# Kernel optimization log

Hardware: AMD Instinct MI355X
Metric: run time of the kernel (lower is better)

Reference implementation:

```python
import jax, jax.numpy as jnp
import numpy as np

B, T, C = 4, 4096, 1024
HEAD_SIZE = 64
HEAD_OUT = 64


def setup_inputs() -> dict:
    key = jax.random.key(0)
    kx, kk, kq, kv = jax.random.split(key, 4)
    x = jax.random.normal(kx, (B, T, C), dtype=jnp.float32)
    # nn.Linear(in, out, bias=False): weight [out, in]; y = x @ W.T
    Wk = jax.random.normal(kk, (HEAD_SIZE, C), dtype=jnp.float32) * (C ** -0.5)
    Wq = jax.random.normal(kq, (HEAD_SIZE, C), dtype=jnp.float32) * (C ** -0.5)
    Wv = jax.random.normal(kv, (HEAD_OUT, C), dtype=jnp.float32) * (C ** -0.5)
    return {"x": x, "Wk": Wk, "Wq": Wq, "Wv": Wv}


def reference(x, Wk, Wq, Wv):
    Tlen = x.shape[1]
    k = jnp.einsum('btc,hc->bth', x, Wk)  # [B,T,Hs]
    q = jnp.einsum('btc,hc->bth', x, Wq)  # [B,T,Hs]
    v = jnp.einsum('btc,oc->bto', x, Wv)  # [B,T,Ho]
    scale = HEAD_SIZE ** -0.5
    scores = jnp.einsum('bih,bjh->bij', q, k) * scale  # [B,T,T]
    # torch.tril(ones, diagonal=1): allowed where j <= i+1 (note: one superdiagonal kept)
    i = jnp.arange(Tlen)[:, None]
    j = jnp.arange(Tlen)[None, :]
    allowed = j <= i + 1
    masked = jnp.where(allowed, scores, -jnp.inf)
    # NOTE: original scales AGAIN inside softmax (double scaling, faithful)
    weights = jax.nn.softmax(masked * scale, axis=-1)
    return jnp.einsum('bij,bjo->bio', weights, v)  # [B,T,Ho]
```

## Files before the change

### kernel.cpp

```cpp
#include <hip/hip_runtime.h>

#define BB 4
#define TT 4096
#define CC 1024
#define HH 64
#define AW 4

typedef unsigned short us;
typedef us v8u __attribute__((ext_vector_type(8)));
typedef us v4u __attribute__((ext_vector_type(4)));
typedef __bf16 v8bf __attribute__((ext_vector_type(8)));
typedef float v4f __attribute__((ext_vector_type(4)));

__device__ __forceinline__ us f2bf(float f) {
  unsigned u = __builtin_bit_cast(unsigned, f);
  u += 0x7fffu + ((u >> 16) & 1u);
  return (us)(u >> 16);
}
__device__ __forceinline__ v8bf ldb(const us* p) {
  return __builtin_bit_cast(v8bf, *(const v8u*)p);
}

__global__ __launch_bounds__(256) void convertw_kernel(const float* __restrict__ Wk,
                                                       const float* __restrict__ Wq,
                                                       const float* __restrict__ Wv,
                                                       us* __restrict__ wpack) {
  const int g = blockIdx.x * 256 + threadIdx.x;
  const int t = g >> 13;
  const int rem = g & 8191;
  const int oc = rem >> 11;
  const int kc = (rem >> 6) & 31;
  const int lane = rem & 63;
  const float* W = (t == 0) ? Wq : ((t == 1) ? Wk : Wv);
  const int h  = oc * 16 + (lane & 15);
  const int d0 = kc * 32 + (lane >> 4) * 8;
  const float4* src = (const float4*)(W + h * CC + d0);
  const float4 f0 = src[0], f1 = src[1];
  v8u o;
  o[0]=f2bf(f0.x); o[1]=f2bf(f0.y); o[2]=f2bf(f0.z); o[3]=f2bf(f0.w);
  o[4]=f2bf(f1.x); o[5]=f2bf(f1.y); o[6]=f2bf(f1.z); o[7]=f2bf(f1.w);
  *(v8u*)(wpack + (size_t)g * 8) = o;
}


__global__ __launch_bounds__(512, 4) void proj_kernel(
    const float* __restrict__ x, const us* __restrict__ wpack,
    us* __restrict__ qpack, us* __restrict__ kpack, us* __restrict__ vpack)
{
  __shared__ __align__(16) float red[3][2][3][4][64][4];

  const int tid  = threadIdx.x;
  const int lane = tid & 63, w = tid >> 6;
  const int i16 = lane & 15, quad = lane >> 4;
  const int rg = w & 1, kq = w >> 1;
  const int rows0 = blockIdx.x * 32;

  const float* xp = x + (size_t)(rows0 + rg * 16 + i16) * CC + kq * 256 + quad * 8;

  v4f zero = {0.f, 0.f, 0.f, 0.f};
  v4f acc[3][4];
  #pragma unroll
  for (int t = 0; t < 3; t++)
    #pragma unroll
    for (int oc = 0; oc < 4; oc++) acc[t][oc] = zero;

  #pragma unroll 2
  for (int kc = 0; kc < 8; kc++) {
    const float4 f0 = *(const float4*)(xp + kc * 32);
    const float4 f1 = *(const float4*)(xp + kc * 32 + 4);
    v8u au;
    au[0]=f2bf(f0.x); au[1]=f2bf(f0.y); au[2]=f2bf(f0.z); au[3]=f2bf(f0.w);
    au[4]=f2bf(f1.x); au[5]=f2bf(f1.y); au[6]=f2bf(f1.z); au[7]=f2bf(f1.w);
    const v8bf a = __builtin_bit_cast(v8bf, au);
    const size_t wo = (size_t)(kq * 8 + kc) * 512 + lane * 8;
    #pragma unroll
    for (int oc = 0; oc < 4; oc++) {
      acc[0][oc] = __builtin_amdgcn_mfma_f32_16x16x32_bf16(a, ldb(wpack + (0*4+oc)*16384 + wo), acc[0][oc], 0, 0, 0);
      acc[1][oc] = __builtin_amdgcn_mfma_f32_16x16x32_bf16(a, ldb(wpack + (1*4+oc)*16384 + wo), acc[1][oc], 0, 0, 0);
      acc[2][oc] = __builtin_amdgcn_mfma_f32_16x16x32_bf16(a, ldb(wpack + (2*4+oc)*16384 + wo), acc[2][oc], 0, 0, 0);
    }
  }

  if (kq) {
    #pragma unroll
    for (int t = 0; t < 3; t++)
      #pragma unroll
      for (int oc = 0; oc < 4; oc++)
        *(v4f*)&red[kq - 1][rg][t][oc][lane][0] = acc[t][oc];
  }
  __syncthreads();

  if (kq == 0) {
    #pragma unroll
    for (int p = 0; p < 3; p++)
      #pragma unroll
      for (int t = 0; t < 3; t++)
        #pragma unroll
        for (int oc = 0; oc < 4; oc++) {
          const v4f pv = *(const v4f*)&red[p][rg][t][oc][lane][0];
          #pragma unroll
          for (int r = 0; r < 4; r++) acc[t][oc][r] += pv[r];
        }

    const float COEF = 0.015625f * 1.4426950408889634f;
    const int b    = (rows0 >> 12);
    const int tile = (rows0 & (TT - 1)) >> 5;

    #pragma unroll
    for (int oc = 0; oc < 4; oc++) {
      const int h = oc * 16 + i16;
      #pragma unroll
      for (int r = 0; r < 4; r++) {
        const int tr = quad * 4 + r;
        const int lane2 = tr + 16 * ((h >> 3) & 3);
        const size_t idx = ((((size_t)(b * 128 + tile) * 2 + rg) * 2 + (h >> 5)) * 64 + lane2) * 8 + (h & 7);
        qpack[idx] = f2bf(acc[0][oc][r] * COEF);
        kpack[idx] = f2bf(acc[1][oc][r]);
      }
      const int lane3 = i16 + 16 * (rg * 2 + (quad >> 1));
      v4u pk;
      #pragma unroll
      for (int r = 0; r < 4; r++) pk[r] = f2bf(acc[2][oc][r]);
      *(v4u*)&vpack[(((size_t)(b * 128 + tile) * 4 + oc) * 64 + lane3) * 8 + (quad & 1) * 4] = pk;
    }
  }
}

__global__ __launch_bounds__(256) void attn_kernel(
    const us* __restrict__ qpack, const us* __restrict__ kpack,
    const us* __restrict__ vpack, float* __restrict__ out)
{
  __shared__ float shbuf[AW][2148];

  const int tid  = threadIdx.x;
  const int lane = tid & 63, warp = tid >> 6;
  const int i16 = lane & 15, quad = lane >> 4;

  const int p = blockIdx.x & 255, s = blockIdx.x >> 8;
  const int b  = p & 3;
  const int q0 = p >> 2;
  const int qb = s ? (127 - q0) : q0;
  const int i0 = qb << 5;
  const int nt = min(qb + 2, 128);

  us* Pw = (us*)shbuf[warp];
  const float NEGINF = -__builtin_inff();

  v8bf qf[2][2];
  #pragma unroll
  for (int ih = 0; ih < 2; ih++)
    #pragma unroll
    for (int g = 0; g < 2; g++)
      qf[ih][g] = ldb(qpack + ((((size_t)(b * 128 + qb) * 2 + ih) * 2 + g) * 64 + lane) * 8);

  v4f zero = {0.f, 0.f, 0.f, 0.f};
  v4f oacc[2][4];
  #pragma unroll
  for (int ih = 0; ih < 2; ih++)
    #pragma unroll
    for (int oc = 0; oc < 4; oc++) oacc[ih][oc] = zero;
  float lsum[2] = {0.f, 0.f};

  auto loadK = [&](int t, v8bf kf[2][2]) {
    #pragma unroll
    for (int f = 0; f < 2; f++)
      #pragma unroll
      for (int g = 0; g < 2; g++)
        kf[f][g] = ldb(kpack + ((((size_t)(b * 128 + t) * 2 + f) * 2 + g) * 64 + lane) * 8);
  };
  auto loadV = [&](int t, v8bf vf[4]) {
    #pragma unroll
    for (int oc = 0; oc < 4; oc++)
      vf[oc] = ldb(vpack + (((size_t)(b * 128 + t) * 4 + oc) * 64 + lane) * 8);
  };
  auto qk_exp_store = [&](int t, const v8bf kf[2][2], int buf) {
    v4f sacc[2][2];
    #pragma unroll
    for (int ih = 0; ih < 2; ih++)
      #pragma unroll
      for (int f = 0; f < 2; f++) {
        v4f sv = zero;
        sv = __builtin_amdgcn_mfma_f32_16x16x32_bf16(kf[f][0], qf[ih][0], sv, 0, 0, 0);
        sv = __builtin_amdgcn_mfma_f32_16x16x32_bf16(kf[f][1], qf[ih][1], sv, 0, 0, 0);
        sacc[ih][f] = sv;
      }
    const int j0 = t * 32;
    const bool needMask = (t >= qb);
    #pragma unroll
    for (int ih = 0; ih < 2; ih++) {
      float ps[8];
      #pragma unroll
      for (int f = 0; f < 2; f++)
        #pragma unroll
        for (int r = 0; r < 4; r++) {
          float sv = fminf(sacc[ih][f][r], 80.f);
          if (needMask) {
            const int j = j0 + f * 16 + quad * 4 + r;
            const int i = i0 + ih * 16 + i16;
            sv = (j <= i + 1) ? sv : NEGINF;
          }
          ps[f * 4 + r] = exp2f(sv);
          lsum[ih] += ps[f * 4 + r];
        }
      #pragma unroll
      for (int f = 0; f < 2; f++) {
        v4u pk;
        #pragma unroll
        for (int r = 0; r < 4; r++) pk[r] = f2bf(ps[f * 4 + r]);
        *(v4u*)&Pw[buf * 1280 + ih * 640 + i16 * 40 + f * 16 + quad * 4] = pk;
      }
    }
  };
  auto pv = [&](int buf, const v8bf vf[4]) {
    #pragma unroll
    for (int ih = 0; ih < 2; ih++) {
      v8bf pf = __builtin_bit_cast(v8bf, *(const v8u*)&Pw[buf * 1280 + ih * 640 + i16 * 40 + quad * 8]);
      #pragma unroll
      for (int oc = 0; oc < 4; oc++)
        oacc[ih][oc] = __builtin_amdgcn_mfma_f32_16x16x32_bf16(vf[oc], pf, oacc[ih][oc], 0, 0, 0);
    }
  };

  int t = warp, buf = 0;
  if (t < nt) {
    v8bf kf[2][2], vprev[4];
    loadK(t, kf); loadV(t, vprev);
    qk_exp_store(t, kf, 0);
    for (t += AW; t < nt; t += AW) {
      v8bf kf2[2][2], vnew[4];
      loadK(t, kf2); loadV(t, vnew);
      pv(buf, vprev);
      qk_exp_store(t, kf2, buf ^ 1);
      #pragma unroll
      for (int v = 0; v < 4; v++) vprev[v] = vnew[v];
      buf ^= 1;
    }
    pv(buf, vprev);
  }

  #pragma unroll
  for (int ih = 0; ih < 2; ih++) {
    lsum[ih] += __shfl_xor(lsum[ih], 16, 64);
    lsum[ih] += __shfl_xor(lsum[ih], 32, 64);
    #pragma unroll
    for (int oc = 0; oc < 4; oc++)
      #pragma unroll
      for (int r = 0; r < 4; r++)
        shbuf[warp][(oc * 16 + quad * 4 + r) * 33 + ih * 16 + i16] = oacc[ih][oc][r];
  }
  if (lane < 16) {
    shbuf[warp][2112 + lane]      = lsum[0];
    shbuf[warp][2112 + 16 + lane] = lsum[1];
  }
  __syncthreads();

  const int o  = tid & 63;
  const int iw = tid >> 6;
  #pragma unroll
  for (int rr = 0; rr < 8; rr++) {
    const int i = iw + rr * 4;
    float L = 0.f, O = 0.f;
    #pragma unroll
    for (int w = 0; w < AW; w++) {
      L += shbuf[w][2112 + i];
      O += shbuf[w][o * 33 + i];
    }
    out[(size_t)(b * TT + i0 + i) * HH + o] = O / L;
  }
}

extern "C" void kernel_launch(void* const* d_in, const int* in_sizes, int n_in,
                              void* d_out, int out_size, void* d_ws, size_t ws_size,
                              hipStream_t stream) {
  const size_t NWP = 3 * 4 * 32 * 64 * 8;
  const size_t NP  = (size_t)BB * TT * HH;

  us* wpack = (us*)d_ws;
  us* qpack = wpack + NWP;
  us* kpack = qpack + NP;
  us* vpack = kpack + NP;
  float* out = (float*)d_out;

  convertw_kernel<<<96, 256, 0, stream>>>(
      (const float*)d_in[1], (const float*)d_in[2], (const float*)d_in[3], wpack);
  proj_kernel<<<BB * TT / 32, 512, 0, stream>>>(
      (const float*)d_in[0], wpack, qpack, kpack, vpack);
  attn_kernel<<<512, 256, 0, stream>>>(qpack, kpack, vpack, out);
}
```

Baseline: 157.4 us.

## Restructure projection to stage x tile in LDS and split outputs across warps

```diff
diff --git a/kernel.cpp b/kernel.cpp
--- a/kernel.cpp
+++ b/kernel.cpp
@@ -43,84 +43,74 @@
 }
 
 
-__global__ __launch_bounds__(512, 4) void proj_kernel(
+__global__ __launch_bounds__(768, 6) void proj_kernel(
     const float* __restrict__ x, const us* __restrict__ wpack,
     us* __restrict__ qpack, us* __restrict__ kpack, us* __restrict__ vpack)
 {
-  __shared__ __align__(16) float red[3][2][3][4][64][4];
+  __shared__ __align__(16) us xlds[64][520];
 
   const int tid  = threadIdx.x;
   const int lane = tid & 63, w = tid >> 6;
   const int i16 = lane & 15, quad = lane >> 4;
-  const int rg = w & 1, kq = w >> 1;
-  const int rows0 = blockIdx.x * 32;
-
-  const float* xp = x + (size_t)(rows0 + rg * 16 + i16) * CC + kq * 256 + quad * 8;
-
+  const int t = w >> 2, oc = w & 3;
+  const int rows0 = blockIdx.x * 64;
+
+  const us* wp = wpack + (size_t)w * 16384 + lane * 8;
   v4f zero = {0.f, 0.f, 0.f, 0.f};
-  v4f acc[3][4];
-  #pragma unroll
-  for (int t = 0; t < 3; t++)
-    #pragma unroll
-    for (int oc = 0; oc < 4; oc++) acc[t][oc] = zero;
-
-  #pragma unroll 2
-  for (int kc = 0; kc < 8; kc++) {
-    const float4 f0 = *(const float4*)(xp + kc * 32);
-    const float4 f1 = *(const float4*)(xp + kc * 32 + 4);
-    v8u au;
-    au[0]=f2bf(f0.x); au[1]=f2bf(f0.y); au[2]=f2bf(f0.z); au[3]=f2bf(f0.w);
-    au[4]=f2bf(f1.x); au[5]=f2bf(f1.y); au[6]=f2bf(f1.z); au[7]=f2bf(f1.w);
-    const v8bf a = __builtin_bit_cast(v8bf, au);
-    const size_t wo = (size_t)(kq * 8 + kc) * 512 + lane * 8;
-    #pragma unroll
-    for (int oc = 0; oc < 4; oc++) {
-      acc[0][oc] = __builtin_amdgcn_mfma_f32_16x16x32_bf16(a, ldb(wpack + (0*4+oc)*16384 + wo), acc[0][oc], 0, 0, 0);
-      acc[1][oc] = __builtin_amdgcn_mfma_f32_16x16x32_bf16(a, ldb(wpack + (1*4+oc)*16384 + wo), acc[1][oc], 0, 0, 0);
-      acc[2][oc] = __builtin_amdgcn_mfma_f32_16x16x32_bf16(a, ldb(wpack + (2*4+oc)*16384 + wo), acc[2][oc], 0, 0, 0);
-    }
-  }
-
-  if (kq) {
-    #pragma unroll
-    for (int t = 0; t < 3; t++)
-      #pragma unroll
-      for (int oc = 0; oc < 4; oc++)
-        *(v4f*)&red[kq - 1][rg][t][oc][lane][0] = acc[t][oc];
-  }
-  __syncthreads();
-
-  if (kq == 0) {
-    #pragma unroll
-    for (int p = 0; p < 3; p++)
-      #pragma unroll
-      for (int t = 0; t < 3; t++)
-        #pragma unroll
-        for (int oc = 0; oc < 4; oc++) {
-          const v4f pv = *(const v4f*)&red[p][rg][t][oc][lane][0];
-          #pragma unroll
-          for (int r = 0; r < 4; r++) acc[t][oc][r] += pv[r];
-        }
-
-    const float COEF = 0.015625f * 1.4426950408889634f;
-    const int b    = (rows0 >> 12);
-    const int tile = (rows0 & (TT - 1)) >> 5;
-
-    #pragma unroll
-    for (int oc = 0; oc < 4; oc++) {
-      const int h = oc * 16 + i16;
+  v4f acc[4] = {zero, zero, zero, zero};
+
+  #pragma unroll
+  for (int ph = 0; ph < 2; ph++) {
+    if (ph) __syncthreads();
+    const float4* xg4 = (const float4*)(x + (size_t)rows0 * CC + ph * 512);
+    for (int i = tid; i < 8192; i += 768) {
+      const int r = i >> 7, c = i & 127;
+      const float4 f = xg4[r * 256 + c];
+      v4u o; o[0]=f2bf(f.x); o[1]=f2bf(f.y); o[2]=f2bf(f.z); o[3]=f2bf(f.w);
+      *(v4u*)&xlds[r][c * 4] = o;
+    }
+    __syncthreads();
+
+    #pragma unroll 4
+    for (int kc = 0; kc < 16; kc++) {
+      const v8bf wf = ldb(wp + (ph * 16 + kc) * 512);
+      #pragma unroll
+      for (int rg = 0; rg < 4; rg++) {
+        const v8bf a = ldb(&xlds[rg * 16 + i16][kc * 32 + quad * 8]);
+        acc[rg] = __builtin_amdgcn_mfma_f32_16x16x32_bf16(a, wf, acc[rg], 0, 0, 0);
+      }
+    }
+  }
+
+  const float COEF = 0.015625f * 1.4426950408889634f;
+  const int b     = rows0 >> 12;
+  const int tile0 = (rows0 & (TT - 1)) >> 5;
+
+  if (t < 2) {
+    us* dst = t ? kpack : qpack;
+    const float c = t ? 1.0f : COEF;
+    const int h = oc * 16 + i16;
+    #pragma unroll
+    for (int rg16 = 0; rg16 < 4; rg16++) {
+      const int tile = tile0 + (rg16 >> 1);
+      const int rg = rg16 & 1;
       #pragma unroll
       for (int r = 0; r < 4; r++) {
         const int tr = quad * 4 + r;
         const int lane2 = tr + 16 * ((h >> 3) & 3);
         const size_t idx = ((((size_t)(b * 128 + tile) * 2 + rg) * 2 + (h >> 5)) * 64 + lane2) * 8 + (h & 7);
-        qpack[idx] = f2bf(acc[0][oc][r] * COEF);
-        kpack[idx] = f2bf(acc[1][oc][r]);
-      }
+        dst[idx] = f2bf(acc[rg16][r] * c);
+      }
+    }
+  } else {
+    #pragma unroll
+    for (int rg16 = 0; rg16 < 4; rg16++) {
+      const int tile = tile0 + (rg16 >> 1);
+      const int rg = rg16 & 1;
       const int lane3 = i16 + 16 * (rg * 2 + (quad >> 1));
       v4u pk;
       #pragma unroll
-      for (int r = 0; r < 4; r++) pk[r] = f2bf(acc[2][oc][r]);
+      for (int r = 0; r < 4; r++) pk[r] = f2bf(acc[rg16][r]);
       *(v4u*)&vpack[(((size_t)(b * 128 + tile) * 4 + oc) * 64 + lane3) * 8 + (quad & 1) * 4] = pk;
     }
   }
@@ -283,7 +273,7 @@
 
   convertw_kernel<<<96, 256, 0, stream>>>(
       (const float*)d_in[1], (const float*)d_in[2], (const float*)d_in[3], wpack);
-  proj_kernel<<<BB * TT / 32, 512, 0, stream>>>(
+  proj_kernel<<<BB * TT / 64, 768, 0, stream>>>(
       (const float*)d_in[0], wpack, qpack, kpack, vpack);
   attn_kernel<<<512, 256, 0, stream>>>(qpack, kpack, vpack, out);
 }
```

After: 146.1 us. -7.2%, faster.
